# Kernel optimization log

Hardware: AMD Instinct MI355X
Metric: run time of the kernel (lower is better)

## Reference

```python
import jax, jax.numpy as jnp
import numpy as np

B, S, H, F, E, TOPK = 2, 2048, 1024, 2048, 8, 2


def setup_inputs() -> dict:
    key = jax.random.key(0)
    k1, k2, k3, k4, k5 = jax.random.split(key, 5)
    scale_h = 1.0 / np.sqrt(H)
    scale_f = 1.0 / np.sqrt(F)
    return {
        "hidden_states": jax.random.normal(k1, (B, S, H), dtype=jnp.float32),
        "gate_w": jax.random.normal(k2, (E, H), dtype=jnp.float32) * scale_h,
        "w1": jax.random.normal(k3, (E, F, H), dtype=jnp.float32) * scale_h,
        "w2": jax.random.normal(k4, (E, H, F), dtype=jnp.float32) * scale_f,
        "w3": jax.random.normal(k5, (E, F, H), dtype=jnp.float32) * scale_h,
    }


def reference(hidden_states, gate_w, w1, w2, w3):
    b, s, h = hidden_states.shape
    x = hidden_states.reshape(-1, h)                      # [T, H]
    T = x.shape[0]
    router_logits = x @ gate_w.T                          # [T, E]
    probs = jax.nn.softmax(router_logits.astype(jnp.float32), axis=-1)
    rw, sel = jax.lax.top_k(probs, TOPK)                  # [T, k]
    rw = rw / jnp.sum(rw, axis=-1, keepdims=True)
    rw = rw.astype(x.dtype)
    # combine weights [T, E]: routing weight where selected, else 0
    combine = jnp.zeros((T, E), dtype=x.dtype).at[
        jnp.arange(T)[:, None], sel].add(rw)
    # dense dispatch: compute every expert on all tokens, mask via combine
    h1 = jnp.einsum('th,efh->etf', x, w1)                 # [E, T, F]
    h3 = jnp.einsum('th,efh->etf', x, w3)
    gated = jax.nn.silu(h1) * h3
    out_e = jnp.einsum('etf,ehf->eth', gated, w2)         # [E, T, H]
    final = jnp.einsum('eth,te->th', out_e, combine)      # [T, H]
    return final.reshape(b, s, h), router_logits
```

## Files before the change

### kernel.cpp

```cpp
#include <hip/hip_runtime.h>
#include <hip/hip_bf16.h>

#define TT 4096
#define HH 1024
#define FF 2048
#define EE 8
#define NC32 2048
#define LDSU 32768

typedef short short8_t __attribute__((ext_vector_type(8)));
typedef float f32x4 __attribute__((ext_vector_type(4)));

__device__ __forceinline__ unsigned short f2b(float f) {
  union { float f; unsigned u; } v; v.f = f;
  return (unsigned short)((v.u + 0x7fffu + ((v.u >> 16) & 1u)) >> 16);
}

__device__ __forceinline__ void gload16(const unsigned short* g, void* l) {
  __builtin_amdgcn_global_load_lds(
      (const __attribute__((address_space(1))) void*)g,
      (__attribute__((address_space(3))) void*)l, 16, 0, 0);
}

#define FENCE asm volatile("" ::: "memory")

__device__ __forceinline__ void conv_ilp(const float* __restrict__ src,
                                         unsigned short* __restrict__ dst,
                                         int c, int tid) {
  size_t base = (size_t)c * 8192 + tid * 4;
  float4 v[8];
#pragma unroll
  for (int j = 0; j < 8; ++j)
    v[j] = *reinterpret_cast<const float4*>(src + base + j * 1024);
#pragma unroll
  for (int j = 0; j < 8; ++j) {
    ushort4 b4;
    b4.x = f2b(v[j].x); b4.y = f2b(v[j].y); b4.z = f2b(v[j].z); b4.w = f2b(v[j].w);
    *reinterpret_cast<ushort4*>(dst + base + j * 1024) = b4;
  }
}

__global__ __launch_bounds__(256) void front_kernel(
    const float* __restrict__ x, const float* __restrict__ gw,
    const float* __restrict__ w1, const float* __restrict__ w3,
    const float* __restrict__ w2,
    float* __restrict__ out_logits,
    unsigned short* __restrict__ xbf,
    unsigned short* __restrict__ w1bf, unsigned short* __restrict__ w3bf,
    unsigned short* __restrict__ w2bf,
    int* __restrict__ sel01, float2* __restrict__ w01)
{
  int tid = threadIdx.x;
  int b = blockIdx.x;
  if (b >= TT) {
    int cb = b - TT;
    if (cb < NC32)          conv_ilp(w1, w1bf, cb, tid);
    else if (cb < 2 * NC32) conv_ilp(w3, w3bf, cb - NC32, tid);
    else                    conv_ilp(w2, w2bf, cb - 2 * NC32, tid);
    return;
  }
  int t = b;

  __shared__ float xs[HH];
  __shared__ float lg[EE];

  float4 v = reinterpret_cast<const float4*>(x + (size_t)t * HH)[tid];
  xs[tid * 4 + 0] = v.x; xs[tid * 4 + 1] = v.y;
  xs[tid * 4 + 2] = v.z; xs[tid * 4 + 3] = v.w;
  ushort4 b4;
  b4.x = f2b(v.x); b4.y = f2b(v.y); b4.z = f2b(v.z); b4.w = f2b(v.w);
  reinterpret_cast<ushort4*>(xbf + (size_t)t * HH)[tid] = b4;
  __syncthreads();

  int lane = tid & 63, wv = tid >> 6;
  for (int e = wv; e < EE; e += 4) {
    float s = 0.f;
    const float* g = gw + (size_t)e * HH;
#pragma unroll
    for (int j = 0; j < HH / 64; ++j) s += xs[lane + j * 64] * g[lane + j * 64];
#pragma unroll
    for (int off = 32; off > 0; off >>= 1) s += __shfl_down(s, off);
    if (lane == 0) lg[e] = s;
  }
  __syncthreads();

  if (tid < 8) out_logits[(size_t)t * EE + tid] = lg[tid];
  if (tid == 0) {
    float l[EE];
#pragma unroll
    for (int e = 0; e < EE; ++e) l[e] = lg[e];
    int e0 = 0;
#pragma unroll
    for (int e = 1; e < EE; ++e) if (l[e] > l[e0]) e0 = e;
    int e1 = -1;
#pragma unroll
    for (int e = 0; e < EE; ++e) if (e != e0 && (e1 < 0 || l[e] > l[e1])) e1 = e;
    float p1 = expf(l[e1] - l[e0]);
    float w0 = 1.f / (1.f + p1);
    float w1v = p1 * w0;
    sel01[t] = e0 | (e1 << 8);
    w01[t] = make_float2(w0, w1v);
  }
}

__global__ __launch_bounds__(256) void build_kernel(
    const int* __restrict__ sel01, const float2* __restrict__ w01,
    int* __restrict__ counts, int* __restrict__ tokidx, float* __restrict__ rww)
{
  int e = blockIdx.x;
  int tid = threadIdx.x, lane = tid & 63, wv = tid >> 6;
  __shared__ int wsum[4];
  int base = 0;
  for (int t0 = 0; t0 < TT; t0 += 256) {
    int t = t0 + tid;
    int s = sel01[t];
    int e0 = s & 255, e1 = (s >> 8) & 255;
    bool hit = (e0 == e) || (e1 == e);
    float w = 0.f;
    if (hit) { float2 ww = w01[t]; w = (e0 == e) ? ww.x : ww.y; }
    unsigned long long m = __ballot(hit);
    int wpre = __popcll(m & ((1ull << lane) - 1));
    if (lane == 63) wsum[wv] = wpre + (hit ? 1 : 0);
    __syncthreads();
    int wbase = base;
    for (int q = 0; q < wv; ++q) wbase += wsum[q];
    if (hit) {
      int pos = wbase + wpre;
      tokidx[e * TT + pos] = t;
      rww[e * TT + pos] = w;
    }
    base += wsum[0] + wsum[1] + wsum[2] + wsum[3];
    __syncthreads();
  }
  if (tid == 0) counts[e] = base;
}

__global__ __launch_bounds__(256) void conv_kernel(
    const float* __restrict__ src, unsigned short* __restrict__ dst)
{
  conv_ilp(src, dst, blockIdx.x, threadIdx.x);
}

__global__ __launch_bounds__(256) void combine_kernel(
    const float4* __restrict__ s0, const float4* __restrict__ s1,
    float4* __restrict__ out)
{
  size_t i = (size_t)blockIdx.x * 256 + threadIdx.x;
  float4 a = s0[i], b = s1[i];
  float4 r;
  r.x = a.x + b.x; r.y = a.y + b.y; r.z = a.z + b.z; r.w = a.w + b.w;
  out[i] = r;
}

__global__ __launch_bounds__(256) void up_gate_kernel(
    const unsigned short* __restrict__ xbf,
    const unsigned short* __restrict__ w1bf, const unsigned short* __restrict__ w3bf,
    const int* __restrict__ counts, const int* __restrict__ tokidx,
    unsigned short* __restrict__ gated)
{
  int e = blockIdx.z;
  int n = counts[e];
  int row0 = blockIdx.y * 128;
  if (row0 >= n) return;
  int fbase = blockIdx.x * 64;

  int pe = 0;
  for (int q = 0; q < e; ++q) pe += (counts[q] + 127) & ~127;

  __shared__ __align__(16) char lds[2 * LDSU];

  int tid = threadIdx.x;
  int lane = tid & 63, wv = tid >> 6;
  int sb = (tid & 7) ^ ((tid >> 3) & 7);

  const unsigned short* ga[4];
#pragma unroll
  for (int j = 0; j < 4; ++j) {
    int r = min(row0 + (tid >> 3) + 32 * j, n - 1);
    ga[j] = xbf + (size_t)tokidx[e * TT + r] * HH + sb * 8;
  }
  const unsigned short* gb1[2];
  const unsigned short* gb3[2];
#pragma unroll
  for (int j = 0; j < 2; ++j) {
    size_t rw_ = (size_t)e * FF + fbase + (tid >> 3) + 32 * j;
    gb1[j] = w1bf + rw_ * HH + sb * 8;
    gb3[j] = w3bf + rw_ * HH + sb * 8;
  }

  int wr = (wv >> 1) * 64, wc = (wv & 1) * 32;
  int fr = lane & 15, kq = lane >> 4, l7 = lane & 7;

  f32x4 acc1[4][2], acc3[4][2];
#pragma unroll
  for (int m = 0; m < 4; ++m)
#pragma unroll
    for (int nn = 0; nn < 2; ++nn) { acc1[m][nn] = (f32x4)0.f; acc3[m][nn] = (f32x4)0.f; }

  short8_t a0[4], b10[2], b30[2];
  short8_t a1[4], b11[2], b31[2];

#define UG_STAGE(T, SOFF) do {                                                     \
    _Pragma("unroll") for (int j = 0; j < 4; ++j)                                  \
      gload16(ga[j] + (T) * 64, lds + (SOFF) + j * 4096 + wv * 1024);              \
    _Pragma("unroll") for (int j = 0; j < 2; ++j) {                                \
      gload16(gb1[j] + (T) * 64, lds + (SOFF) + 16384 + j * 4096 + wv * 1024);     \
      gload16(gb3[j] + (T) * 64, lds + (SOFF) + 24576 + j * 4096 + wv * 1024);     \
    } } while (0)

#define UG_READS(SOFF, KS, A_, B1_, B3_) do {                                               \
    int bswz = (((KS) * 4 + kq) ^ l7) * 16;                                                 \
    _Pragma("unroll") for (int m = 0; m < 4; ++m)                                           \
      A_[m] = *(const short8_t*)(lds + (SOFF) + (wr + m * 16 + fr) * 128 + bswz);           \
    _Pragma("unroll") for (int nn = 0; nn < 2; ++nn) {                                      \
      B1_[nn] = *(const short8_t*)(lds + (SOFF) + 16384 + (wc + nn * 16 + fr) * 128 + bswz); \
      B3_[nn] = *(const short8_t*)(lds + (SOFF) + 24576 + (wc + nn * 16 + fr) * 128 + bswz); \
    } } while (0)

#define UG_MFMA(A_, B1_, B3_) do {                                                          \
    __builtin_amdgcn_s_setprio(1);                                                          \
    _Pragma("unroll") for (int m = 0; m < 4; ++m)                                           \
      _Pragma("unroll") for (int nn = 0; nn < 2; ++nn) {                                    \
        acc1[m][nn] = __builtin_amdgcn_mfma_f32_16x16x32_bf16(A_[m], B1_[nn], acc1[m][nn], 0, 0, 0); \
        acc3[m][nn] = __builtin_amdgcn_mfma_f32_16x16x32_bf16(A_[m], B3_[nn], acc3[m][nn], 0, 0, 0); \
      }                                                                                     \
    __builtin_amdgcn_s_setprio(0);                                                          \
  } while (0)

#define UG_WAITS do {                                                  \
    asm volatile("s_waitcnt lgkmcnt(0) vmcnt(0)" ::: "memory");        \
    __builtin_amdgcn_sched_barrier(0);                                 \
    __builtin_amdgcn_s_barrier(); FENCE;                               \
  } while (0)

#define UG_NT 16
  UG_STAGE(0, 0);
  UG_STAGE(1, LDSU);
  asm volatile("s_waitcnt vmcnt(8)" ::: "memory");
  __builtin_amdgcn_s_barrier(); FENCE;
  UG_READS(0, 0, a0, b10, b30);

  for (int t2 = 0; t2 < UG_NT; t2 += 2) {
    UG_READS(0, 1, a1, b11, b31);
    UG_MFMA(a0, b10, b30);
    UG_WAITS;
    if (t2 + 2 < UG_NT) UG_STAGE(t2 + 2, 0);
    UG_READS(LDSU, 0, a0, b10, b30);
    UG_MFMA(a1, b11, b31);
    UG_READS(LDSU, 1, a1, b11, b31);
    UG_MFMA(a0, b10, b30);
    UG_WAITS;
    if (t2 + 3 < UG_NT) UG_STAGE(t2 + 3, LDSU);
    if (t2 + 2 < UG_NT) UG_READS(0, 0, a0, b10, b30);
    UG_MFMA(a1, b11, b31);
  }
#undef UG_STAGE
#undef UG_READS
#undef UG_MFMA
#undef UG_WAITS

  size_t gbase = ((size_t)pe + row0) * FF + fbase;
#pragma unroll
  for (int m = 0; m < 4; ++m) {
#pragma unroll
    for (int nn = 0; nn < 2; ++nn) {
      f32x4 h1v = acc1[m][nn], h3v = acc3[m][nn];
#pragma unroll
      for (int j = 0; j < 4; ++j) {
        float z = h1v[j];
        float val = (z / (1.f + expf(-z))) * h3v[j];
        int r = wr + m * 16 + (lane >> 4) * 4 + j;
        int c = wc + nn * 16 + fr;
        gated[gbase + (size_t)r * FF + c] = f2b(val);
      }
    }
  }
}

__global__ __launch_bounds__(256) void down_kernel(
    const unsigned short* __restrict__ gated,
    const unsigned short* __restrict__ w2bf,
    const int* __restrict__ counts, const int* __restrict__ tokidx,
    const float* __restrict__ rww, const int* __restrict__ sel01,
    float* __restrict__ slots)
{
  int e = blockIdx.z;
  int n = counts[e];
  int row0 = blockIdx.y * 128;
  if (row0 >= n) return;
  int hbase = blockIdx.x * 128;
  int valid = min(128, n - row0);

  int pe = 0;
  for (int q = 0; q < e; ++q) pe += (counts[q] + 127) & ~127;

  __shared__ __align__(16) char lds[2 * LDSU];

  int tid = threadIdx.x;
  int lane = tid & 63, wv = tid >> 6;
  int sb = (tid & 7) ^ ((tid >> 3) & 7);

  const unsigned short* ga[4];
  const unsigned short* gb[4];
#pragma unroll
  for (int j = 0; j < 4; ++j) {
    ga[j] = gated + ((size_t)pe + row0 + (tid >> 3) + 32 * j) * FF + sb * 8;
    gb[j] = w2bf + ((size_t)e * HH + hbase + (tid >> 3) + 32 * j) * FF + sb * 8;
  }

  int wr = (wv >> 1) * 64, wc = (wv & 1) * 64;
  int fr = lane & 15, kq = lane >> 4, l7 = lane & 7;

  f32x4 acc[4][4];
#pragma unroll
  for (int m = 0; m < 4; ++m)
#pragma unroll
    for (int nn = 0; nn < 4; ++nn) acc[m][nn] = (f32x4)0.f;

  short8_t a0[4], bf0[4];
  short8_t a1[4], bf1[4];

#define DN_STAGE(T, SOFF) do {                                                   \
    _Pragma("unroll") for (int j = 0; j < 4; ++j) {                              \
      gload16(ga[j] + (T) * 64, lds + (SOFF) + j * 4096 + wv * 1024);            \
      gload16(gb[j] + (T) * 64, lds + (SOFF) + 16384 + j * 4096 + wv * 1024);    \
    } } while (0)

#define DN_READS(SOFF, KS, A_, B_) do {                                                    \
    int bswz = (((KS) * 4 + kq) ^ l7) * 16;                                                \
    _Pragma("unroll") for (int m = 0; m < 4; ++m)                                          \
      A_[m] = *(const short8_t*)(lds + (SOFF) + (wr + m * 16 + fr) * 128 + bswz);          \
    _Pragma("unroll") for (int nn = 0; nn < 4; ++nn)                                       \
      B_[nn] = *(const short8_t*)(lds + (SOFF) + 16384 + (wc + nn * 16 + fr) * 128 + bswz); \
  } while (0)

#define DN_MFMA(A_, B_) do {                                                               \
    __builtin_amdgcn_s_setprio(1);                                                         \
    _Pragma("unroll") for (int m = 0; m < 4; ++m)                                          \
      _Pragma("unroll") for (int nn = 0; nn < 4; ++nn)                                     \
        acc[m][nn] = __builtin_amdgcn_mfma_f32_16x16x32_bf16(A_[m], B_[nn], acc[m][nn], 0, 0, 0); \
    __builtin_amdgcn_s_setprio(0);                                                         \
  } while (0)

#define DN_WAITS do {                                                  \
    asm volatile("s_waitcnt lgkmcnt(0) vmcnt(0)" ::: "memory");        \
    __builtin_amdgcn_sched_barrier(0);                                 \
    __builtin_amdgcn_s_barrier(); FENCE;                               \
  } while (0)

#define DN_NT 32
  DN_STAGE(0, 0);
  DN_STAGE(1, LDSU);
  asm volatile("s_waitcnt vmcnt(8)" ::: "memory");
  __builtin_amdgcn_s_barrier(); FENCE;
  DN_READS(0, 0, a0, bf0);

  for (int t2 = 0; t2 < DN_NT; t2 += 2) {
    DN_READS(0, 1, a1, bf1);
    DN_MFMA(a0, bf0);
    DN_WAITS;
    if (t2 + 2 < DN_NT) DN_STAGE(t2 + 2, 0);
    DN_READS(LDSU, 0, a0, bf0);
    DN_MFMA(a1, bf1);

    DN_READS(LDSU, 1, a1, bf1);
    DN_MFMA(a0, bf0);
    DN_WAITS;
    if (t2 + 3 < DN_NT) DN_STAGE(t2 + 3, LDSU);
    if (t2 + 2 < DN_NT) DN_READS(0, 0, a0, bf0);
    DN_MFMA(a1, bf1);
  }
#undef DN_STAGE
#undef DN_READS
#undef DN_MFMA
#undef DN_WAITS

#pragma unroll
  for (int m = 0; m < 4; ++m) {
    int rbase = wr + m * 16 + (lane >> 4) * 4;
#pragma unroll
    for (int j = 0; j < 4; ++j) {
      int r = rbase + j;
      if (r < valid) {
        int t = tokidx[e * TT + row0 + r];
        float w = rww[e * TT + row0 + r];
        int sl = ((sel01[t] & 255) == e) ? 0 : 1;
        float* dst = slots + (size_t)sl * TT * HH + (size_t)t * HH;
#pragma unroll
        for (int nn = 0; nn < 4; ++nn) {
          int c = hbase + wc + nn * 16 + fr;
          dst[c] = w * acc[m][nn][j];
        }
      }
    }
  }
}

extern "C" void kernel_launch(void* const* d_in, const int* in_sizes, int n_in,
                              void* d_out, int out_size, void* d_ws, size_t ws_size,
                              hipStream_t stream) {
  const float* x  = (const float*)d_in[0];
  const float* gw = (const float*)d_in[1];
  const float* w1 = (const float*)d_in[2];
  const float* w2 = (const float*)d_in[3];
  const float* w3 = (const float*)d_in[4];

  float* final_out  = (float*)d_out;
  float* out_logits = final_out + (size_t)TT * HH;

  char* ws = (char*)d_ws;
  int*    counts = (int*)(ws + 0);
  int*    sel01  = (int*)(ws + 1024);
  float2* w01    = (float2*)(ws + 20480);
  int*    tokidx = (int*)(ws + 53248);
  float*  rww    = (float*)(ws + 184320);
  unsigned short* xbf   = (unsigned short*)(ws + 315392);
  unsigned short* w1bf  = (unsigned short*)(ws + 8704000);
  unsigned short* w3bf  = (unsigned short*)(ws + 42258432);
  unsigned short* gated = (unsigned short*)(ws + 75812864);
  const size_t base_end = 113561600;
  bool big = ws_size >= base_end + 33554432;
  unsigned short* w2bf = big ? (unsigned short*)(ws + base_end) : w1bf;
  float* slots = (float*)w3bf;

  int nconvblk = (big ? 3 : 2) * NC32;
  front_kernel<<<TT + nconvblk, 256, 0, stream>>>(
      x, gw, w1, w3, w2, out_logits, xbf, w1bf, w3bf, w2bf, sel01, w01);
  build_kernel<<<EE, 256, 0, stream>>>(sel01, w01, counts, tokidx, rww);
  up_gate_kernel<<<dim3(FF / 64, TT / 128, EE), 256, 0, stream>>>(
      xbf, w1bf, w3bf, counts, tokidx, gated);
  if (!big) conv_kernel<<<NC32, 256, 0, stream>>>(w2, w1bf);
  down_kernel<<<dim3(HH / 128, TT / 128, EE), 256, 0, stream>>>(
      gated, w2bf, counts, tokidx, rww, sel01, slots);
  combine_kernel<<<TT * HH / 1024, 256, 0, stream>>>(
      (const float4*)slots, (const float4*)(slots + (size_t)TT * HH),
      (float4*)final_out);
}
```

Baseline: 249.5 us.

## Enlarge up-gate tile to 256x128 with 512 threads and ping-pong schedule

Changes the up/gate GEMM kernel from 128x64 tiles on 256 threads to 256x128 tiles on 512 threads (8 waves), with 128KB of dynamic LDS double-buffered. The K loop is restructured into a barrier-interleaved schedule: staging of A and B halves is split across MFMA phases, and acc1 and acc3 are updated in separate blocks. Larger tiles raise arithmetic intensity and reduce redundant loads of x and the weights. In exchange, occupancy and scheduling flexibility drop, more barriers are added, and padded rows beyond the 128-aligned count are now masked on store.

```diff
diff --git a/kernel.cpp b/kernel.cpp
--- a/kernel.cpp
+++ b/kernel.cpp
@@ -7,6 +7,7 @@
 #define EE 8
 #define NC32 2048
 #define LDSU 32768
+#define UGSL 65536
 
 typedef short short8_t __attribute__((ext_vector_type(8)));
 typedef float f32x4 __attribute__((ext_vector_type(4)));
@@ -152,7 +153,7 @@
   out[i] = r;
 }
 
-__global__ __launch_bounds__(256) void up_gate_kernel(
+__global__ __launch_bounds__(512, 2) void up_gate_kernel(
     const unsigned short* __restrict__ xbf,
     const unsigned short* __restrict__ w1bf, const unsigned short* __restrict__ w3bf,
     const int* __restrict__ counts, const int* __restrict__ tokidx,
@@ -160,14 +161,15 @@
 {
   int e = blockIdx.z;
   int n = counts[e];
-  int row0 = blockIdx.y * 128;
+  int row0 = blockIdx.y * 256;
   if (row0 >= n) return;
-  int fbase = blockIdx.x * 64;
+  int fbase = blockIdx.x * 128;
 
   int pe = 0;
   for (int q = 0; q < e; ++q) pe += (counts[q] + 127) & ~127;
-
-  __shared__ __align__(16) char lds[2 * LDSU];
+  int prows = (n + 127) & ~127;
+
+  extern __shared__ __align__(16) char lds[];
 
   int tid = threadIdx.x;
   int lane = tid & 63, wv = tid >> 6;
@@ -176,102 +178,113 @@
   const unsigned short* ga[4];
 #pragma unroll
   for (int j = 0; j < 4; ++j) {
-    int r = min(row0 + (tid >> 3) + 32 * j, n - 1);
+    int r = min(row0 + (tid >> 3) + 64 * j, n - 1);
     ga[j] = xbf + (size_t)tokidx[e * TT + r] * HH + sb * 8;
   }
   const unsigned short* gb1[2];
   const unsigned short* gb3[2];
 #pragma unroll
   for (int j = 0; j < 2; ++j) {
-    size_t rw_ = (size_t)e * FF + fbase + (tid >> 3) + 32 * j;
+    size_t rw_ = (size_t)e * FF + fbase + (tid >> 3) + 64 * j;
     gb1[j] = w1bf + rw_ * HH + sb * 8;
     gb3[j] = w3bf + rw_ * HH + sb * 8;
   }
 
-  int wr = (wv >> 1) * 64, wc = (wv & 1) * 32;
+  int wr = (wv >> 1) * 64;
+  int wcc = (wv & 1) * 64;
   int fr = lane & 15, kq = lane >> 4, l7 = lane & 7;
 
-  f32x4 acc1[4][2], acc3[4][2];
+  f32x4 acc1[4][4], acc3[4][4];
 #pragma unroll
   for (int m = 0; m < 4; ++m)
 #pragma unroll
-    for (int nn = 0; nn < 2; ++nn) { acc1[m][nn] = (f32x4)0.f; acc3[m][nn] = (f32x4)0.f; }
-
-  short8_t a0[4], b10[2], b30[2];
-  short8_t a1[4], b11[2], b31[2];
-
-#define UG_STAGE(T, SOFF) do {                                                     \
-    _Pragma("unroll") for (int j = 0; j < 4; ++j)                                  \
-      gload16(ga[j] + (T) * 64, lds + (SOFF) + j * 4096 + wv * 1024);              \
-    _Pragma("unroll") for (int j = 0; j < 2; ++j) {                                \
-      gload16(gb1[j] + (T) * 64, lds + (SOFF) + 16384 + j * 4096 + wv * 1024);     \
-      gload16(gb3[j] + (T) * 64, lds + (SOFF) + 24576 + j * 4096 + wv * 1024);     \
+    for (int nn = 0; nn < 4; ++nn) { acc1[m][nn] = (f32x4)0.f; acc3[m][nn] = (f32x4)0.f; }
+
+  short8_t aa0[4], aa1[4], bb1a[4], bb1b[4], bb3a[4], bb3b[4];
+
+#define UG_STAGE_H0(T, SOFF) do {                                        \
+    _Pragma("unroll") for (int j = 0; j < 4; ++j)                        \
+      gload16(ga[j] + (T) * 64, lds + (SOFF) + j * 8192 + wv * 1024);    \
+  } while (0)
+#define UG_STAGE_H1(T, SOFF) do {                                        \
+    _Pragma("unroll") for (int j = 0; j < 2; ++j) {                      \
+      gload16(gb1[j] + (T) * 64, lds + (SOFF) + 32768 + j * 8192 + wv * 1024); \
+      gload16(gb3[j] + (T) * 64, lds + (SOFF) + 49152 + j * 8192 + wv * 1024); \
     } } while (0)
 
 #define UG_READS(SOFF, KS, A_, B1_, B3_) do {                                               \
     int bswz = (((KS) * 4 + kq) ^ l7) * 16;                                                 \
     _Pragma("unroll") for (int m = 0; m < 4; ++m)                                           \
       A_[m] = *(const short8_t*)(lds + (SOFF) + (wr + m * 16 + fr) * 128 + bswz);           \
-    _Pragma("unroll") for (int nn = 0; nn < 2; ++nn) {                                      \
-      B1_[nn] = *(const short8_t*)(lds + (SOFF) + 16384 + (wc + nn * 16 + fr) * 128 + bswz); \
-      B3_[nn] = *(const short8_t*)(lds + (SOFF) + 24576 + (wc + nn * 16 + fr) * 128 + bswz); \
+    _Pragma("unroll") for (int nn = 0; nn < 4; ++nn) {                                      \
+      B1_[nn] = *(const short8_t*)(lds + (SOFF) + 32768 + (wcc + nn * 16 + fr) * 128 + bswz); \
+      B3_[nn] = *(const short8_t*)(lds + (SOFF) + 49152 + (wcc + nn * 16 + fr) * 128 + bswz); \
     } } while (0)
 
-#define UG_MFMA(A_, B1_, B3_) do {                                                          \
+#define UG_MM(ACC, A_, B_) do {                                                             \
     __builtin_amdgcn_s_setprio(1);                                                          \
     _Pragma("unroll") for (int m = 0; m < 4; ++m)                                           \
-      _Pragma("unroll") for (int nn = 0; nn < 2; ++nn) {                                    \
-        acc1[m][nn] = __builtin_amdgcn_mfma_f32_16x16x32_bf16(A_[m], B1_[nn], acc1[m][nn], 0, 0, 0); \
-        acc3[m][nn] = __builtin_amdgcn_mfma_f32_16x16x32_bf16(A_[m], B3_[nn], acc3[m][nn], 0, 0, 0); \
-      }                                                                                     \
+      _Pragma("unroll") for (int nn = 0; nn < 4; ++nn)                                      \
+        ACC[m][nn] = __builtin_amdgcn_mfma_f32_16x16x32_bf16(A_[m], B_[nn], ACC[m][nn], 0, 0, 0); \
     __builtin_amdgcn_s_setprio(0);                                                          \
   } while (0)
 
-#define UG_WAITS do {                                                  \
-    asm volatile("s_waitcnt lgkmcnt(0) vmcnt(0)" ::: "memory");        \
-    __builtin_amdgcn_sched_barrier(0);                                 \
-    __builtin_amdgcn_s_barrier(); FENCE;                               \
-  } while (0)
-
 #define UG_NT 16
-  UG_STAGE(0, 0);
-  UG_STAGE(1, LDSU);
+#define UG_TILE(T, SOFF) do {                                            \
+                                         \
+    UG_READS(SOFF, 0, aa0, bb1a, bb3a);                                  \
+    __builtin_amdgcn_s_barrier(); FENCE;                                 \
+    UG_MM(acc1, aa0, bb1a);                                              \
+    FENCE; __builtin_amdgcn_s_barrier(); FENCE;                          \
+                                         \
+    UG_READS(SOFF, 1, aa1, bb1b, bb3b);                                  \
+    __builtin_amdgcn_s_barrier(); FENCE;                                 \
+    UG_MM(acc3, aa0, bb3a);                                              \
+    asm volatile("s_waitcnt lgkmcnt(0)" ::: "memory");                   \
+    __builtin_amdgcn_sched_barrier(0);                                   \
+    __builtin_amdgcn_s_barrier(); FENCE;                                 \
+       \
+    if ((T) + 2 < UG_NT) UG_STAGE_H0((T) + 2, SOFF);                     \
+    __builtin_amdgcn_s_barrier(); FENCE;                                 \
+    UG_MM(acc1, aa1, bb1b);                                              \
+    FENCE; __builtin_amdgcn_s_barrier(); FENCE;                          \
+                 \
+    if ((T) + 2 < UG_NT) UG_STAGE_H1((T) + 2, SOFF);                     \
+    __builtin_amdgcn_s_barrier(); FENCE;                                 \
+    UG_MM(acc3, aa1, bb3b);                                              \
+    if ((T) + 1 < UG_NT) asm volatile("s_waitcnt vmcnt(8)" ::: "memory"); \
+    else                 asm volatile("s_waitcnt vmcnt(0)" ::: "memory"); \
+    __builtin_amdgcn_sched_barrier(0);                                   \
+    __builtin_amdgcn_s_barrier(); FENCE;                                 \
+  } while (0)
+
+  UG_STAGE_H0(0, 0);     UG_STAGE_H1(0, 0);
+  UG_STAGE_H0(1, UGSL);  UG_STAGE_H1(1, UGSL);
   asm volatile("s_waitcnt vmcnt(8)" ::: "memory");
   __builtin_amdgcn_s_barrier(); FENCE;
-  UG_READS(0, 0, a0, b10, b30);
-
-  for (int t2 = 0; t2 < UG_NT; t2 += 2) {
-    UG_READS(0, 1, a1, b11, b31);
-    UG_MFMA(a0, b10, b30);
-    UG_WAITS;
-    if (t2 + 2 < UG_NT) UG_STAGE(t2 + 2, 0);
-    UG_READS(LDSU, 0, a0, b10, b30);
-    UG_MFMA(a1, b11, b31);
-    UG_READS(LDSU, 1, a1, b11, b31);
-    UG_MFMA(a0, b10, b30);
-    UG_WAITS;
-    if (t2 + 3 < UG_NT) UG_STAGE(t2 + 3, LDSU);
-    if (t2 + 2 < UG_NT) UG_READS(0, 0, a0, b10, b30);
-    UG_MFMA(a1, b11, b31);
-  }
-#undef UG_STAGE
+
+  for (int t2 = 0; t2 < UG_NT; t2 += 2) { UG_TILE(t2, 0); UG_TILE(t2 + 1, UGSL); }
+#undef UG_STAGE_H0
+#undef UG_STAGE_H1
 #undef UG_READS
-#undef UG_MFMA
-#undef UG_WAITS
+#undef UG_MM
+#undef UG_TILE
 
   size_t gbase = ((size_t)pe + row0) * FF + fbase;
 #pragma unroll
   for (int m = 0; m < 4; ++m) {
 #pragma unroll
-    for (int nn = 0; nn < 2; ++nn) {
+    for (int nn = 0; nn < 4; ++nn) {
       f32x4 h1v = acc1[m][nn], h3v = acc3[m][nn];
 #pragma unroll
       for (int j = 0; j < 4; ++j) {
-        float z = h1v[j];
-        float val = (z / (1.f + expf(-z))) * h3v[j];
-        int r = wr + m * 16 + (lane >> 4) * 4 + j;
-        int c = wc + nn * 16 + fr;
-        gated[gbase + (size_t)r * FF + c] = f2b(val);
+        int r = wr + m * 16 + kq * 4 + j;
+        if (row0 + r < prows) {
+          float z = h1v[j];
+          float val = (z / (1.f + expf(-z))) * h3v[j];
+          int c = wcc + nn * 16 + fr;
+          gated[gbase + (size_t)r * FF + c] = f2b(val);
+        }
       }
     }
   }
@@ -427,7 +440,7 @@
   front_kernel<<<TT + nconvblk, 256, 0, stream>>>(
       x, gw, w1, w3, w2, out_logits, xbf, w1bf, w3bf, w2bf, sel01, w01);
   build_kernel<<<EE, 256, 0, stream>>>(sel01, w01, counts, tokidx, rww);
-  up_gate_kernel<<<dim3(FF / 64, TT / 128, EE), 256, 0, stream>>>(
+  up_gate_kernel<<<dim3(FF / 128, TT / 256, EE), 512, 2 * UGSL, stream>>>(
       xbf, w1bf, w3bf, counts, tokidx, gated);
   if (!big) conv_kernel<<<NC32, 256, 0, stream>>>(w2, w1bf);
   down_kernel<<<dim3(HH / 128, TT / 128, EE), 256, 0, stream>>>(
```

Result: slower. 418.5 us (+67.7%).
